# Performance work log

Hardware: AMD Instinct MI355X
Metric: run time of the kernel (lower is better)

## Reference

```python
import jax, jax.numpy as jnp
import numpy as np

B, S, D, H = 2, 2048, 1024, 16
HD = D // H  # head_dim = 64

def setup_inputs() -> dict:
    key = jax.random.key(0)
    ks = jax.random.split(key, 5)
    scale = 1.0 / np.sqrt(D)
    x = jax.random.normal(ks[0], (B, S, D), dtype=jnp.float32)
    Wq = jax.random.normal(ks[1], (D, D), dtype=jnp.float32) * scale
    Wk = jax.random.normal(ks[2], (D, D), dtype=jnp.float32) * scale
    Wv = jax.random.normal(ks[3], (D, D), dtype=jnp.float32) * scale
    Wf = jax.random.normal(ks[4], (D, D), dtype=jnp.float32) * scale
    z = jnp.zeros((D,), dtype=jnp.float32)
    return {"x": x, "Wq": Wq, "bq": z, "Wk": Wk, "bk": z, "Wv": Wv, "bv": z, "Wf": Wf, "bf": z}

def reference(x, Wq, bq, Wk, bk, Wv, bv, Wf, bf):
    # Linear layers follow torch convention: y = x @ W.T + b
    def split_heads(t):  # [B,S,D] -> [B,H,S,HD]
        return t.reshape(B, S, H, HD).transpose(0, 2, 1, 3)
    q = split_heads(x @ Wq.T + bq)
    k = split_heads(x @ Wk.T + bk)
    v = split_heads(x @ Wv.T + bv)
    scores = jnp.einsum('bhqd,bhkd->bhqk', q, k) / jnp.sqrt(jnp.float32(HD))
    causal = jnp.tril(jnp.ones((S, S), dtype=bool))  # [S,S]
    scores = jnp.where(causal[None, None], scores, -jnp.inf)
    attn = jax.nn.softmax(scores, axis=-1)
    out = jnp.einsum('bhqk,bhkd->bhqd', attn, v)
    out = out.transpose(0, 2, 1, 3).reshape(B, S, D)
    return out @ Wf.T + bf
```

## Files before the change

### kernel.cpp

```cpp
#include <hip/hip_runtime.h>
#include <stdint.h>

#define B_  2
#define S_  2048
#define D_  1024
#define H_  16
#define HD_ 64
#define M_  (B_*S_)

typedef __bf16 bf16x8 __attribute__((ext_vector_type(8)));
typedef float  f32x4  __attribute__((ext_vector_type(4)));

typedef const __attribute__((address_space(1))) void* gas_ptr;
typedef __attribute__((address_space(3))) void* las_ptr;

__device__ __forceinline__ uint16_t f32_to_bf16(float f) {
  uint32_t u = __float_as_uint(f);
  u += 0x7FFFu + ((u >> 16) & 1u);
  return (uint16_t)(u >> 16);
}

__device__ __forceinline__ void g2l16(const uint16_t* g, uint16_t* l) {
  __builtin_amdgcn_global_load_lds((gas_ptr)g, (las_ptr)l, 16, 0, 0);
}

__device__ __forceinline__ int swz_src(int s) {
  return (s >> 2) * D_ + (((s & 3) ^ ((s >> 3) & 3)) * 8);
}

__global__ void cast_all(const float* __restrict__ x,
                         const float* __restrict__ wq, const float* __restrict__ wk,
                         const float* __restrict__ wv, const float* __restrict__ wf,
                         uint16_t* __restrict__ xb,
                         uint16_t* __restrict__ wqb, uint16_t* __restrict__ wkb,
                         uint16_t* __restrict__ wvb, uint16_t* __restrict__ wfb) {
  const int X4 = M_ * D_ / 4;
  const int W4 = D_ * D_ / 4;
  int i = blockIdx.x * 256 + threadIdx.x;
  const float* src; uint16_t* dst; int off;
  if (i < X4) { src = x; dst = xb; off = i; }
  else {
    int j = i - X4;
    int w = j >> 18;
    off = j & (W4 - 1);
    src = (w == 0) ? wq : (w == 1) ? wk : (w == 2) ? wv : wf;
    dst = (w == 0) ? wqb : (w == 1) ? wkb : (w == 2) ? wvb : wfb;
  }
  float4 v = ((const float4*)src)[off];
  ushort4 o;
  o.x = f32_to_bf16(v.x); o.y = f32_to_bf16(v.y);
  o.z = f32_to_bf16(v.z); o.w = f32_to_bf16(v.w);
  ((ushort4*)dst)[off] = o;
}

__device__ __forceinline__ void gemm_tile_128_bk64(
    const uint16_t* __restrict__ A, const uint16_t* __restrict__ B,
    int am0, int bn0, uint16_t* As, uint16_t* Bs, f32x4 (&acc)[4][4])
{
  const int tid  = threadIdx.x;
  const int wave = tid >> 6;
  const int lane = tid & 63;
  const int quad = lane >> 4;
  const int l16  = lane & 15;
  const int wm = (wave >> 1) * 64;
  const int wn = (wave & 1) * 64;
  const int sw = quad ^ ((l16 >> 1) & 3);

  #pragma unroll
  for (int i = 0; i < 4; ++i)
    #pragma unroll
    for (int j = 0; j < 4; ++j)
      #pragma unroll
      for (int e = 0; e < 4; ++e)
        acc[i][j][e] = 0.f;

  const int s0 = wave * 64 + lane;
  const int s1 = s0 + 256;
  const int so0 = swz_src(s0), so1 = swz_src(s1);
  uint16_t* lA0 = As + (size_t)(wave * 64) * 8;
  uint16_t* lA1 = As + (size_t)(256 + wave * 64) * 8;
  uint16_t* lB0 = Bs + (size_t)(wave * 64) * 8;
  uint16_t* lB1 = Bs + (size_t)(256 + wave * 64) * 8;
  const uint16_t* gA0 = A + (size_t)am0 * D_ + so0;
  const uint16_t* gA1 = A + (size_t)am0 * D_ + so1;
  const uint16_t* gB0 = B + (size_t)bn0 * D_ + so0;
  const uint16_t* gB1 = B + (size_t)bn0 * D_ + so1;

  for (int k0 = 0; k0 < D_; k0 += 64) {
    g2l16(gA0 + k0,      lA0);
    g2l16(gA1 + k0,      lA1);
    g2l16(gB0 + k0,      lB0);
    g2l16(gB1 + k0,      lB1);
    g2l16(gA0 + k0 + 32, lA0 + 4096);
    g2l16(gA1 + k0 + 32, lA1 + 4096);
    g2l16(gB0 + k0 + 32, lB0 + 4096);
    g2l16(gB1 + k0 + 32, lB1 + 4096);
    __syncthreads();
    bf16x8 af0[4], af1[4], bf0[4], bf1[4];
    #pragma unroll
    for (int mt = 0; mt < 4; ++mt) {
      const int ro = ((wm + mt * 16 + l16) * 4 + sw) * 8;
      af0[mt] = *(const bf16x8*)(As + ro);
      af1[mt] = *(const bf16x8*)(As + 4096 + ro);
    }
    #pragma unroll
    for (int nt = 0; nt < 4; ++nt) {
      const int ro = ((wn + nt * 16 + l16) * 4 + sw) * 8;
      bf0[nt] = *(const bf16x8*)(Bs + ro);
      bf1[nt] = *(const bf16x8*)(Bs + 4096 + ro);
    }
    #pragma unroll
    for (int mt = 0; mt < 4; ++mt)
      #pragma unroll
      for (int nt = 0; nt < 4; ++nt) {
        acc[mt][nt] = __builtin_amdgcn_mfma_f32_16x16x32_bf16(
            af0[mt], bf0[nt], acc[mt][nt], 0, 0, 0);
        acc[mt][nt] = __builtin_amdgcn_mfma_f32_16x16x32_bf16(
            af1[mt], bf1[nt], acc[mt][nt], 0, 0, 0);
      }
    __syncthreads();
  }
}

__global__ __launch_bounds__(256)
void qkv_gemm(const uint16_t* __restrict__ xb,
              const uint16_t* __restrict__ wqb, const uint16_t* __restrict__ wkb,
              const uint16_t* __restrict__ wvb,
              const float* __restrict__ bqv, const float* __restrict__ bkv,
              const float* __restrict__ bvv,
              uint16_t* __restrict__ qout, uint16_t* __restrict__ kout,
              uint16_t* __restrict__ vtout)
{
  __shared__ __align__(16) uint16_t As[2 * 128 * 32];
  __shared__ __align__(16) uint16_t Bs[2 * 128 * 32];
  const int wsel = blockIdx.x >> 3;
  const int nsel = blockIdx.x & 7;
  const int mtile = blockIdx.y;
  const int lane = threadIdx.x & 63, wave = threadIdx.x >> 6;
  const int quad = lane >> 4, l16 = lane & 15;
  const int wm = (wave >> 1) * 64, wn = (wave & 1) * 64;

  const uint16_t *Ap, *Bp;
  int m0e, n0e;
  if (wsel < 2) {
    Ap = xb; Bp = (wsel == 0) ? wqb : wkb;
    m0e = mtile * 128; n0e = nsel * 128;
  } else {
    Ap = wvb; Bp = xb;
    m0e = nsel * 128; n0e = mtile * 128;
  }
  f32x4 acc[4][4];
  gemm_tile_128_bk64(Ap, Bp, m0e, n0e, As, Bs, acc);

  if (wsel < 2) {
    const float* bias = (wsel == 0) ? bqv : bkv;
    uint16_t* outp = (wsel == 0) ? qout : kout;
    const float scl = (wsel == 0) ? 0.18033688f : 1.0f;
    #pragma unroll
    for (int nt = 0; nt < 4; ++nt) {
      const int n = n0e + wn + nt * 16 + l16;
      const int h = n >> 6, hd = n & 63;
      const float bia = bias[n];
      #pragma unroll
      for (int mt = 0; mt < 4; ++mt) {
        #pragma unroll
        for (int r = 0; r < 4; ++r) {
          const int m = m0e + wm + mt * 16 + quad * 4 + r;
          const int bb = m >> 11, s = m & (S_ - 1);
          outp[(((size_t)(bb * H_ + h)) * S_ + s) * HD_ + hd] =
              f32_to_bf16((acc[mt][nt][r] + bia) * scl);
        }
      }
    }
  } else {
    #pragma unroll
    for (int mt = 0; mt < 4; ++mt) {
      #pragma unroll
      for (int r = 0; r < 4; ++r) {
        const int m = m0e + wm + mt * 16 + quad * 4 + r;
        const int h = m >> 6, hd = m & 63;
        const float bia = bvv[m];
        #pragma unroll
        for (int nt = 0; nt < 4; ++nt) {
          const int n = n0e + wn + nt * 16 + l16;
          const int bb = n >> 11, s = n & (S_ - 1);
          vtout[(((size_t)(bb * H_ + h)) * HD_ + hd) * S_ + s] =
              f32_to_bf16(acc[mt][nt][r] + bia);
        }
      }
    }
  }
}

__global__ __launch_bounds__(256)
void flash_attn(const uint16_t* __restrict__ qb, const uint16_t* __restrict__ kb,
                const uint16_t* __restrict__ vtb, uint16_t* __restrict__ ao)
{
  __shared__ __align__(16) uint16_t ks[2][64 * 32];
  __shared__ __align__(16) uint16_t vs[2][64 * 32];
  __shared__ __align__(16) uint16_t p_lds[4][16][72];

  const int bh = blockIdx.x;
  const int qt = (int)(gridDim.y - 1u - blockIdx.y);
  const int wave = threadIdx.x >> 6, lane = threadIdx.x & 63;
  const int quad = lane >> 4, l16 = lane & 15;
  const int sw = quad ^ ((l16 >> 1) & 3);
  const int q0 = qt * 64;

  const uint16_t* Q  = qb  + (size_t)bh * S_ * HD_;
  const uint16_t* Kp = kb  + (size_t)bh * S_ * HD_;
  const uint16_t* Vt = vtb + (size_t)bh * HD_ * S_;

  const int qrow = q0 + wave * 16;
  bf16x8 aq0 = *(const bf16x8*)(Q + (size_t)(qrow + l16) * HD_ + quad * 8);
  bf16x8 aq1 = *(const bf16x8*)(Q + (size_t)(qrow + l16) * HD_ + 32 + quad * 8);

  const int srow = lane >> 2;
  const int schk = (lane & 3) ^ ((lane >> 3) & 3);
  const uint16_t* sb[4]; uint16_t* sdst[4]; int sstep[4];
  #pragma unroll
  for (int j = 0; j < 4; ++j) {
    const int g = wave * 4 + j;
    if (g < 8) {
      const int c = (g >> 2) & 1, rb = g & 3;
      sdst[j] = &ks[c][rb * 512];
      sb[j] = Kp + (size_t)(rb * 16 + srow) * HD_ + c * 32 + schk * 8;
      sstep[j] = 64 * HD_;
    } else {
      const int gg = g - 8, c = (gg >> 2) & 1, rb = gg & 3;
      sdst[j] = &vs[c][rb * 512];
      sb[j] = Vt + (size_t)(rb * 16 + srow) * S_ + c * 32 + schk * 8;
      sstep[j] = 64;
    }
  }

  float lpart[4];
  f32x4 o[4];
  #pragma unroll
  for (int r = 0; r < 4; ++r) lpart[r] = 0.f;
  #pragma unroll
  for (int t = 0; t < 4; ++t)
    #pragma unroll
    for (int e = 0; e < 4; ++e) o[t][e] = 0.f;

  const int rowid = qrow + quad * 4;

  for (int kt = 0; kt <= qt; ++kt) {
    const int kbase = kt * 64;
    const bool diag = (kt == qt);

    #pragma unroll
    for (int j = 0; j < 4; ++j) {
      g2l16(sb[j], sdst[j]);
      sb[j] += sstep[j];
    }
    __syncthreads();

    bf16x8 kf0[4], kf1[4];
    #pragma unroll
    for (int nt = 0; nt < 4; ++nt) {
      kf0[nt] = *(const bf16x8*)(&ks[0][((nt * 16 + l16) * 4 + sw) * 8]);
      kf1[nt] = *(const bf16x8*)(&ks[1][((nt * 16 + l16) * 4 + sw) * 8]);
    }
    f32x4 sacc[4];
    #pragma unroll
    for (int nt = 0; nt < 4; ++nt) {
      #pragma unroll
      for (int e = 0; e < 4; ++e) sacc[nt][e] = 0.f;
      sacc[nt] = __builtin_amdgcn_mfma_f32_16x16x32_bf16(aq0, kf0[nt], sacc[nt], 0, 0, 0);
      sacc[nt] = __builtin_amdgcn_mfma_f32_16x16x32_bf16(aq1, kf1[nt], sacc[nt], 0, 0, 0);
    }

    bf16x8 vf0[4], vf1[4];
    #pragma unroll
    for (int t = 0; t < 4; ++t) {
      vf0[t] = *(const bf16x8*)(&vs[0][((t * 16 + l16) * 4 + sw) * 8]);
      vf1[t] = *(const bf16x8*)(&vs[1][((t * 16 + l16) * 4 + sw) * 8]);
    }

    #pragma unroll
    for (int nt = 0; nt < 4; ++nt) {
      const int kkc = kbase + nt * 16 + l16;
      #pragma unroll
      for (int r = 0; r < 4; ++r) {
        float p = __builtin_amdgcn_exp2f(sacc[nt][r]);
        if (diag && (kkc > rowid + r)) p = 0.f;
        lpart[r] += p;
        p_lds[wave][quad * 4 + r][nt * 16 + l16] = f32_to_bf16(p);
      }
    }

    bf16x8 ap0 = *(const bf16x8*)(&p_lds[wave][l16][quad * 8]);
    bf16x8 ap1 = *(const bf16x8*)(&p_lds[wave][l16][32 + quad * 8]);
    #pragma unroll
    for (int t = 0; t < 4; ++t) {
      o[t] = __builtin_amdgcn_mfma_f32_16x16x32_bf16(ap0, vf0[t], o[t], 0, 0, 0);
      o[t] = __builtin_amdgcn_mfma_f32_16x16x32_bf16(ap1, vf1[t], o[t], 0, 0, 0);
    }
    __syncthreads();
  }

  #pragma unroll
  for (int r = 0; r < 4; ++r) {
    lpart[r] += __shfl_xor(lpart[r], 1, 64);
    lpart[r] += __shfl_xor(lpart[r], 2, 64);
    lpart[r] += __shfl_xor(lpart[r], 4, 64);
    lpart[r] += __shfl_xor(lpart[r], 8, 64);
  }
  const int bb = bh >> 4, h = bh & 15;
  #pragma unroll
  for (int t = 0; t < 4; ++t) {
    #pragma unroll
    for (int r = 0; r < 4; ++r) {
      const float ov = o[t][r] / lpart[r];
      ao[((size_t)(bb * S_ + rowid + r)) * D_ + h * HD_ + t * 16 + l16] =
          f32_to_bf16(ov);
    }
  }
}

__global__ __launch_bounds__(256)
void out_gemm(const uint16_t* __restrict__ ab, const uint16_t* __restrict__ wfb,
              const float* __restrict__ bfv, float* __restrict__ out)
{
  __shared__ __align__(16) uint16_t As[64 * 32];
  __shared__ __align__(16) uint16_t Bs[128 * 32];
  const int m0 = blockIdx.y * 64;
  const int n0 = blockIdx.x * 128;
  const int lane = threadIdx.x & 63, wave = threadIdx.x >> 6;
  const int quad = lane >> 4, l16 = lane & 15;
  const int wm = (wave >> 1) * 32, wn = (wave & 1) * 64;
  const int sw = quad ^ ((l16 >> 1) & 3);

  f32x4 acc[2][4];
  #pragma unroll
  for (int i = 0; i < 2; ++i)
    #pragma unroll
    for (int j = 0; j < 4; ++j)
      #pragma unroll
      for (int e = 0; e < 4; ++e)
        acc[i][j][e] = 0.f;

  const int sA  = wave * 64 + lane;
  const int sB1 = sA + 256;
  uint16_t* lA  = As + (size_t)(wave * 64) * 8;
  uint16_t* lB0 = Bs + (size_t)(wave * 64) * 8;
  uint16_t* lB1 = Bs + (size_t)(256 + wave * 64) * 8;
  const uint16_t* gA  = ab  + (size_t)m0 * D_ + swz_src(sA);
  const uint16_t* gB0 = wfb + (size_t)n0 * D_ + swz_src(sA);
  const uint16_t* gB1 = wfb + (size_t)n0 * D_ + swz_src(sB1);

  for (int k0 = 0; k0 < D_; k0 += 32) {
    g2l16(gA  + k0, lA);
    g2l16(gB0 + k0, lB0);
    g2l16(gB1 + k0, lB1);
    __syncthreads();
    bf16x8 af[2], bfr[4];
    #pragma unroll
    for (int mt = 0; mt < 2; ++mt)
      af[mt] = *(const bf16x8*)(As + ((wm + mt * 16 + l16) * 4 + sw) * 8);
    #pragma unroll
    for (int nt = 0; nt < 4; ++nt)
      bfr[nt] = *(const bf16x8*)(Bs + ((wn + nt * 16 + l16) * 4 + sw) * 8);
    #pragma unroll
    for (int mt = 0; mt < 2; ++mt)
      #pragma unroll
      for (int nt = 0; nt < 4; ++nt)
        acc[mt][nt] = __builtin_amdgcn_mfma_f32_16x16x32_bf16(
            af[mt], bfr[nt], acc[mt][nt], 0, 0, 0);
    __syncthreads();
  }

  #pragma unroll
  for (int nt = 0; nt < 4; ++nt) {
    const int n = n0 + wn + nt * 16 + l16;
    const float bia = bfv[n];
    #pragma unroll
    for (int mt = 0; mt < 2; ++mt) {
      #pragma unroll
      for (int r = 0; r < 4; ++r) {
        const int m = m0 + wm + mt * 16 + quad * 4 + r;
        out[(size_t)m * D_ + n] = acc[mt][nt][r] + bia;
      }
    }
  }
}

extern "C" void kernel_launch(void* const* d_in, const int* in_sizes, int n_in,
                              void* d_out, int out_size, void* d_ws, size_t ws_size,
                              hipStream_t stream) {
  (void)in_sizes; (void)n_in; (void)out_size; (void)ws_size;
  const float* x  = (const float*)d_in[0];
  const float* Wq = (const float*)d_in[1];
  const float* bq = (const float*)d_in[2];
  const float* Wk = (const float*)d_in[3];
  const float* bk = (const float*)d_in[4];
  const float* Wv = (const float*)d_in[5];
  const float* bv = (const float*)d_in[6];
  const float* Wf = (const float*)d_in[7];
  const float* bf = (const float*)d_in[8];
  float* out = (float*)d_out;

  uint16_t* ws = (uint16_t*)d_ws;
  uint16_t* xb   = ws;
  uint16_t* wqb  = xb  + (size_t)M_ * D_;
  uint16_t* wkb  = wqb + (size_t)D_ * D_;
  uint16_t* wvb  = wkb + (size_t)D_ * D_;
  uint16_t* wfb  = wvb + (size_t)D_ * D_;
  uint16_t* qbuf = wfb + (size_t)D_ * D_;
  uint16_t* kbuf = qbuf + (size_t)M_ * D_;
  uint16_t* vtb  = kbuf + (size_t)M_ * D_;
  uint16_t* aob  = vtb  + (size_t)M_ * D_;

  const int CAST_BLOCKS = (M_ * D_ / 4 + 4 * (D_ * D_ / 4)) / 256;
  cast_all<<<CAST_BLOCKS, 256, 0, stream>>>(x, Wq, Wk, Wv, Wf,
                                            xb, wqb, wkb, wvb, wfb);

  qkv_gemm<<<dim3(24, 32), 256, 0, stream>>>(xb, wqb, wkb, wvb, bq, bk, bv,
                                             qbuf, kbuf, vtb);
  flash_attn<<<dim3(32, 32), 256, 0, stream>>>(qbuf, kbuf, vtb, aob);
  out_gemm<<<dim3(8, 64), 256, 0, stream>>>(aob, wfb, bf, out);
}
```

Measured before the change: 188.2 us.

## Widen flash attention key tile to 128 and use truncating bf16 cast for P

The attention inner loop now processes 128 keys per iteration instead of 64, halving the number of loop trips and the __syncthreads barriers per query tile. K and V staging buffers and the P scratch are enlarged to match, and each wave issues eight async global-to-LDS loads per step. The probability-to-bf16 conversion switches from round-to-nearest to truncation to save ALU work. Tradeoffs are more LDS per block, which may reduce occupancy, slightly less accurate P values, and extra masked work on the diagonal when qt is even.

```diff
diff --git a/kernel.cpp b/kernel.cpp
--- a/kernel.cpp
+++ b/kernel.cpp
@@ -18,6 +18,10 @@
   uint32_t u = __float_as_uint(f);
   u += 0x7FFFu + ((u >> 16) & 1u);
   return (uint16_t)(u >> 16);
+}
+
+__device__ __forceinline__ uint16_t f32_to_bf16_rtz(float f) {
+  return (uint16_t)(__float_as_uint(f) >> 16);
 }
 
 __device__ __forceinline__ void g2l16(const uint16_t* g, uint16_t* l) {
@@ -196,9 +200,9 @@
 void flash_attn(const uint16_t* __restrict__ qb, const uint16_t* __restrict__ kb,
                 const uint16_t* __restrict__ vtb, uint16_t* __restrict__ ao)
 {
-  __shared__ __align__(16) uint16_t ks[2][64 * 32];
-  __shared__ __align__(16) uint16_t vs[2][64 * 32];
-  __shared__ __align__(16) uint16_t p_lds[4][16][72];
+  __shared__ __align__(16) uint16_t ks[2][128 * 32];
+  __shared__ __align__(16) uint16_t vs[4][64 * 32];
+  __shared__ __align__(16) uint16_t p_lds[4][16][136];
 
   const int bh = blockIdx.x;
   const int qt = (int)(gridDim.y - 1u - blockIdx.y);
@@ -217,20 +221,20 @@
 
   const int srow = lane >> 2;
   const int schk = (lane & 3) ^ ((lane >> 3) & 3);
-  const uint16_t* sb[4]; uint16_t* sdst[4]; int sstep[4];
-  #pragma unroll
-  for (int j = 0; j < 4; ++j) {
-    const int g = wave * 4 + j;
-    if (g < 8) {
-      const int c = (g >> 2) & 1, rb = g & 3;
+  const uint16_t* sb[8]; uint16_t* sdst[8]; int sstep[8];
+  #pragma unroll
+  for (int j = 0; j < 8; ++j) {
+    const int g = wave * 8 + j;
+    if (g < 16) {
+      const int c = g >> 3, rb = g & 7;
       sdst[j] = &ks[c][rb * 512];
       sb[j] = Kp + (size_t)(rb * 16 + srow) * HD_ + c * 32 + schk * 8;
-      sstep[j] = 64 * HD_;
+      sstep[j] = 128 * HD_;
     } else {
-      const int gg = g - 8, c = (gg >> 2) & 1, rb = gg & 3;
+      const int gg = g - 16, c = gg >> 2, rb = gg & 3;
       sdst[j] = &vs[c][rb * 512];
       sb[j] = Vt + (size_t)(rb * 16 + srow) * S_ + c * 32 + schk * 8;
-      sstep[j] = 64;
+      sstep[j] = 128;
     }
   }
 
@@ -244,58 +248,51 @@
     for (int e = 0; e < 4; ++e) o[t][e] = 0.f;
 
   const int rowid = qrow + quad * 4;
-
-  for (int kt = 0; kt <= qt; ++kt) {
-    const int kbase = kt * 64;
-    const bool diag = (kt == qt);
-
-    #pragma unroll
-    for (int j = 0; j < 4; ++j) {
+  const int nkt2 = (qt >> 1) + 1;
+
+  for (int kt2 = 0; kt2 < nkt2; ++kt2) {
+    const int kbase = kt2 * 128;
+    const bool diag = (kt2 == nkt2 - 1);
+
+    #pragma unroll
+    for (int j = 0; j < 8; ++j) {
       g2l16(sb[j], sdst[j]);
       sb[j] += sstep[j];
     }
     __syncthreads();
 
-    bf16x8 kf0[4], kf1[4];
-    #pragma unroll
-    for (int nt = 0; nt < 4; ++nt) {
-      kf0[nt] = *(const bf16x8*)(&ks[0][((nt * 16 + l16) * 4 + sw) * 8]);
-      kf1[nt] = *(const bf16x8*)(&ks[1][((nt * 16 + l16) * 4 + sw) * 8]);
-    }
-    f32x4 sacc[4];
-    #pragma unroll
-    for (int nt = 0; nt < 4; ++nt) {
+    f32x4 sacc[8];
+    #pragma unroll
+    for (int nt = 0; nt < 8; ++nt) {
+      const int ro = ((nt * 16 + l16) * 4 + sw) * 8;
+      bf16x8 kf0 = *(const bf16x8*)(&ks[0][ro]);
+      bf16x8 kf1 = *(const bf16x8*)(&ks[1][ro]);
       #pragma unroll
       for (int e = 0; e < 4; ++e) sacc[nt][e] = 0.f;
-      sacc[nt] = __builtin_amdgcn_mfma_f32_16x16x32_bf16(aq0, kf0[nt], sacc[nt], 0, 0, 0);
-      sacc[nt] = __builtin_amdgcn_mfma_f32_16x16x32_bf16(aq1, kf1[nt], sacc[nt], 0, 0, 0);
-    }
-
-    bf16x8 vf0[4], vf1[4];
-    #pragma unroll
-    for (int t = 0; t < 4; ++t) {
-      vf0[t] = *(const bf16x8*)(&vs[0][((t * 16 + l16) * 4 + sw) * 8]);
-      vf1[t] = *(const bf16x8*)(&vs[1][((t * 16 + l16) * 4 + sw) * 8]);
-    }
-
-    #pragma unroll
-    for (int nt = 0; nt < 4; ++nt) {
+      sacc[nt] = __builtin_amdgcn_mfma_f32_16x16x32_bf16(aq0, kf0, sacc[nt], 0, 0, 0);
+      sacc[nt] = __builtin_amdgcn_mfma_f32_16x16x32_bf16(aq1, kf1, sacc[nt], 0, 0, 0);
+    }
+
+    #pragma unroll
+    for (int nt = 0; nt < 8; ++nt) {
       const int kkc = kbase + nt * 16 + l16;
       #pragma unroll
       for (int r = 0; r < 4; ++r) {
         float p = __builtin_amdgcn_exp2f(sacc[nt][r]);
         if (diag && (kkc > rowid + r)) p = 0.f;
         lpart[r] += p;
-        p_lds[wave][quad * 4 + r][nt * 16 + l16] = f32_to_bf16(p);
-      }
-    }
-
-    bf16x8 ap0 = *(const bf16x8*)(&p_lds[wave][l16][quad * 8]);
-    bf16x8 ap1 = *(const bf16x8*)(&p_lds[wave][l16][32 + quad * 8]);
-    #pragma unroll
-    for (int t = 0; t < 4; ++t) {
-      o[t] = __builtin_amdgcn_mfma_f32_16x16x32_bf16(ap0, vf0[t], o[t], 0, 0, 0);
-      o[t] = __builtin_amdgcn_mfma_f32_16x16x32_bf16(ap1, vf1[t], o[t], 0, 0, 0);
+        p_lds[wave][quad * 4 + r][nt * 16 + l16] = f32_to_bf16_rtz(p);
+      }
+    }
+
+    #pragma unroll
+    for (int c = 0; c < 4; ++c) {
+      bf16x8 ap = *(const bf16x8*)(&p_lds[wave][l16][c * 32 + quad * 8]);
+      #pragma unroll
+      for (int t = 0; t < 4; ++t) {
+        bf16x8 vf = *(const bf16x8*)(&vs[c][((t * 16 + l16) * 4 + sw) * 8]);
+        o[t] = __builtin_amdgcn_mfma_f32_16x16x32_bf16(ap, vf, o[t], 0, 0, 0);
+      }
     }
     __syncthreads();
   }
```

Result: no change. 189.5 us (+0.7%).
